# Kernel optimization log

Measured on AMD Instinct MI355X. Metric: run time of the kernel, lower is better.

Reference implementation:

```python
import jax, jax.numpy as jnp
import numpy as np


def setup_inputs() -> dict:
    key = jax.random.key(0)
    k1, k2, k3, k4, k5 = jax.random.split(key, 5)
    B, T, H = 32, 4096, 256
    D = 2 * H  # encoder feature dim
    hidden = jax.random.normal(k1, (B, D), dtype=jnp.float32)
    encoder_outputs = jax.random.normal(k2, (B, T, D), dtype=jnp.float32)
    # torch nn.Linear(4H, H): weight [H, 4H], bias [H]
    W_attn = jax.random.normal(k3, (H, 4 * H), dtype=jnp.float32) * (1.0 / np.sqrt(4 * H))
    b_attn = jax.random.normal(k4, (H,), dtype=jnp.float32) * 0.01
    v = jax.random.uniform(k5, (H,), dtype=jnp.float32)  # torch.rand init
    return {"hidden": hidden, "encoder_outputs": encoder_outputs,
            "W_attn": W_attn, "b_attn": b_attn, "v": v}


def reference(hidden, encoder_outputs, W_attn, b_attn, v):
    D = hidden.shape[-1]  # 2*H
    # Split Linear(4H->H) weight into the hidden part and encoder part so we
    # never materialize the [B,T,4H] concat: cat(h,e) @ W.T == h @ Wh.T + e @ We.T
    W_h = W_attn[:, :D]   # [H, 2H]
    W_e = W_attn[:, D:]   # [H, 2H]
    h_proj = hidden @ W_h.T                     # [B, H]
    e_proj = jnp.einsum('btd,hd->bth', encoder_outputs, W_e)  # [B, T, H]
    energy = jnp.tanh(h_proj[:, None, :] + e_proj + b_attn)   # [B, T, H]
    scores = energy @ v                          # [B, T]
    attn_weights = jax.nn.softmax(scores, axis=1)  # softmax over timesteps
    context = jnp.einsum('bt,btd->bd', attn_weights, encoder_outputs)  # [B, 2H]
    return context, attn_weights
```

## Files before the change

kernel.cpp:

```cpp
#include <hip/hip_runtime.h>
#include <hip/hip_bf16.h>
#include <math.h>

#define B_  32
#define T_  4096
#define H_  256
#define D_  512

#define WS_PRE    0
#define WS_WEHI   32768
#define WS_P      294912
#define WS_ML     819200
#define WS_PCTX   827392

using short8  = __attribute__((ext_vector_type(8))) short;
using float4v = __attribute__((ext_vector_type(4))) float;

__device__ __forceinline__ unsigned cvt2_bf16(float lo, float hi) {
    union { __hip_bfloat162 h; unsigned u; } cv;
    cv.h = __float22bfloat162_rn(make_float2(lo, hi));
    return cv.u;
}
__device__ __forceinline__ short8 cvt8_bf16(const float* a) {
    union { unsigned u[4]; short8 s; } r;
    r.u[0] = cvt2_bf16(a[0], a[1]);
    r.u[1] = cvt2_bf16(a[2], a[3]);
    r.u[2] = cvt2_bf16(a[4], a[5]);
    r.u[3] = cvt2_bf16(a[6], a[7]);
    return r.s;
}

__device__ __forceinline__ float fast_tanh(float x) {
    float e = __expf(2.0f * x);
    return 1.0f - 2.0f * __builtin_amdgcn_rcpf(e + 1.0f);
}

__global__ __launch_bounds__(256)
void prep_kernel(const float* __restrict__ hidden,
                 const float* __restrict__ W_attn,
                 const float* __restrict__ b_attn,
                 unsigned char* __restrict__ ws) {
    int blk = blockIdx.x;
    int tid = threadIdx.x;
    if (blk < 32) {
        int b = blk, h = tid;
        const float4* hv = (const float4*)(hidden + b * D_);
        const float4* wv = (const float4*)(W_attn + (size_t)h * 1024);
        float s = 0.f;
        #pragma unroll 4
        for (int d4 = 0; d4 < D_ / 4; ++d4) {
            float4 a = hv[d4], w = wv[d4];
            s += a.x * w.x + a.y * w.y + a.z * w.z + a.w * w.w;
        }
        ((float*)(ws + WS_PRE))[b * H_ + h] = s + b_attn[h];
    } else {
        int q = (blk - 32) * 256 + tid;
        unsigned short* whi = (unsigned short*)(ws + WS_WEHI);
        #pragma unroll
        for (int i = 0; i < 4; ++i) {
            int idx4 = q + i * 8192;
            int n = idx4 >> 7, k = (idx4 & 127) << 2;
            int t = k >> 5, kin = k & 31;
            int quad = kin >> 3, e = kin & 7;
            int slot = quad ^ ((n >> 1) & 3);
            float4 w = *(const float4*)(W_attn + (size_t)n * 1024 + 512 + k);
            unsigned lo = cvt2_bf16(w.x, w.y);
            unsigned hi = cvt2_bf16(w.z, w.w);
            unsigned short* dst = whi + t * 8192 + n * 32 + slot * 8 + e;
            *(uint2*)dst = make_uint2(lo, hi);
        }
    }
}

#define BM 128
#define BN 256
#define BK 32
#define LDT 40
#define KIT 16

__global__ __launch_bounds__(512, 4)
void gemm_scores_kernel(const float* __restrict__ enc,
                        unsigned char* __restrict__ ws,
                        const float* __restrict__ v) {
    __shared__ unsigned short sA[2][BM * LDT];
    __shared__ unsigned short sB[2][BN * BK];
    __shared__ float sScore[BM];
    __shared__ float sP[BM];
    __shared__ float sRed[4];

    const float*          pre = (const float*)(ws + WS_PRE);
    const unsigned short* weh = (const unsigned short*)(ws + WS_WEHI);

    int tid = threadIdx.x;
    int m0  = blockIdx.x * BM;
    int b   = m0 >> 12;

    if (tid < BM) sScore[tid] = 0.f;

    int rowA = tid & 127, cgA = tid >> 7;
    const float* gA = enc + (size_t)(m0 + rowA) * D_ + cgA * 8;

    int wave = tid >> 6, lane = tid & 63;
    int wm = wave & 1, wn = wave >> 1;
    int quad = lane >> 4, l16 = lane & 15;

    float4v acc[4][4] = {};

    float aX[8], aY[8];

    {
        const float4* p0 = (const float4*)gA;
        float4 x0 = p0[0], x1 = p0[1];
        const uint4* pb0 = (const uint4*)weh;
        uint4 t0 = pb0[tid], t1 = pb0[tid + 512];
        const float4* p1 = (const float4*)(gA + BK);
        float4 y0 = p1[0], y1 = p1[1];

        float tmp[8];
        *(float4*)tmp = x0; *(float4*)(tmp + 4) = x1;
        *(short8*)&sA[0][rowA * LDT + cgA * 8] = cvt8_bf16(tmp);
        ((uint4*)sB[0])[tid]       = t0;
        ((uint4*)sB[0])[tid + 512] = t1;
        *(float4*)aY = y0; *(float4*)(aY + 4) = y1;
    }
    __builtin_amdgcn_s_waitcnt(0xc07f);
    __builtin_amdgcn_s_barrier();

#define K_STEP(kk, CUR, NXT, Acons, Aload)                                    \
    {                                                                         \
        uint4 br0, br1;                                                       \
        if ((kk) + 1 < KIT) {                                                 \
            const uint4* pb = (const uint4*)(weh + ((kk) + 1) * 8192);        \
            br0 = pb[tid]; br1 = pb[tid + 512];                               \
        }                                                                     \
        if ((kk) + 2 < KIT) {                                                 \
            const float4* pa = (const float4*)(gA + ((kk) + 2) * BK);         \
            *(float4*)(Aload) = pa[0]; *(float4*)((Aload) + 4) = pa[1];       \
        }                                                                     \
        short8 ah[4], bh[4];                                                  \
        _Pragma("unroll")                                                     \
        for (int i = 0; i < 4; ++i) {                                         \
            int r = wm * 64 + i * 16 + l16;                                   \
            ah[i] = *(const short8*)&sA[CUR][r * LDT + quad * 8];             \
        }                                                                     \
        _Pragma("unroll")                                                     \
        for (int j = 0; j < 4; ++j) {                                         \
            int c = wn * 64 + j * 16 + l16;                                   \
            int slot = quad ^ ((c >> 1) & 3);                                 \
            bh[j] = *(const short8*)&sB[CUR][c * 32 + slot * 8];              \
        }                                                                     \
        _Pragma("unroll")                                                     \
        for (int i = 0; i < 4; ++i)                                           \
            _Pragma("unroll")                                                 \
            for (int j = 0; j < 4; ++j)                                       \
                acc[i][j] = __builtin_amdgcn_mfma_f32_16x16x32_bf16(          \
                    ah[i], bh[j], acc[i][j], 0, 0, 0);                        \
        if ((kk) + 1 < KIT) {                                                 \
            *(short8*)&sA[NXT][rowA * LDT + cgA * 8] = cvt8_bf16(Acons);      \
            ((uint4*)sB[NXT])[tid]       = br0;                               \
            ((uint4*)sB[NXT])[tid + 512] = br1;                               \
            __builtin_amdgcn_s_waitcnt(0xc07f);                               \
            __builtin_amdgcn_s_barrier();                                     \
        }                                                                     \
    }

    for (int kt = 0; kt < 8; ++kt) {
        K_STEP(2 * kt,     0, 1, aY, aX)
        K_STEP(2 * kt + 1, 1, 0, aX, aY)
    }
#undef K_STEP

    float rowsum[4][4] = {};
    #pragma unroll
    for (int j = 0; j < 4; ++j) {
        int n = wn * 64 + j * 16 + l16;
        float pv = pre[b * H_ + n];
        float vv = v[n];
        #pragma unroll
        for (int i = 0; i < 4; ++i)
            #pragma unroll
            for (int r = 0; r < 4; ++r)
                rowsum[i][r] += fast_tanh(acc[i][j][r] + pv) * vv;
    }
    #pragma unroll
    for (int i = 0; i < 4; ++i)
        #pragma unroll
        for (int r = 0; r < 4; ++r) {
            float s = rowsum[i][r];
            s += __shfl_xor(s, 1);
            s += __shfl_xor(s, 2);
            s += __shfl_xor(s, 4);
            s += __shfl_xor(s, 8);
            rowsum[i][r] = s;
        }
    if (l16 == 0) {
        #pragma unroll
        for (int i = 0; i < 4; ++i)
            #pragma unroll
            for (int r = 0; r < 4; ++r) {
                int row = wm * 64 + i * 16 + quad * 4 + r;
                atomicAdd(&sScore[row], rowsum[i][r]);
            }
    }
    __syncthreads();

    if (tid < 128) {
        float s = sScore[tid];
        float m = s;
        #pragma unroll
        for (int off = 32; off; off >>= 1) m = fmaxf(m, __shfl_xor(m, off));
        if (lane == 0) sRed[wave] = m;
    }
    __syncthreads();
    float m_blk = fmaxf(sRed[0], sRed[1]);
    if (tid < 128) {
        float p = expf(sScore[tid] - m_blk);
        sP[tid] = p;
        ((float*)(ws + WS_P))[m0 + tid] = p;
        float l = p;
        #pragma unroll
        for (int off = 32; off; off >>= 1) l += __shfl_xor(l, off);
        if (lane == 0) sRed[2 + wave] = l;
    }
    __syncthreads();
    if (tid == 0) {
        float2 ml = make_float2(m_blk, sRed[2] + sRed[3]);
        ((float2*)(ws + WS_ML))[blockIdx.x] = ml;
    }

    int colg = tid & 127, rgrp = tid >> 7;
    const float* encb = enc + (size_t)m0 * D_;
    float4 c4 = {0.f, 0.f, 0.f, 0.f};
    #pragma unroll 4
    for (int s = 0; s < 32; ++s) {
        int r = rgrp + 4 * s;
        float w = sP[r];
        float4 ev = *(const float4*)(encb + (size_t)r * D_ + colg * 4);
        c4.x += w * ev.x; c4.y += w * ev.y;
        c4.z += w * ev.z; c4.w += w * ev.w;
    }
    float4* red4 = (float4*)sA;
    red4[tid] = c4;
    __syncthreads();
    if (rgrp == 0) {
        float4 a0 = red4[colg], a1 = red4[colg + 128];
        float4 a2 = red4[colg + 256], a3 = red4[colg + 384];
        float4 o;
        o.x = a0.x + a1.x + a2.x + a3.x;
        o.y = a0.y + a1.y + a2.y + a3.y;
        o.z = a0.z + a1.z + a2.z + a3.z;
        o.w = a0.w + a1.w + a2.w + a3.w;
        ((float4*)(ws + WS_PCTX))[blockIdx.x * 128 + colg] = o;
    }
}

__global__ __launch_bounds__(512)
void finalize_kernel(const unsigned char* __restrict__ ws,
                     float* __restrict__ out_ctx,
                     float* __restrict__ out_w) {
    __shared__ float sm[32], sl[32], sscale[32];
    int b = blockIdx.x, tid = threadIdx.x;
    const float2* ml  = ((const float2*)(ws + WS_ML)) + b * 32;
    if (tid < 32) {
        float2 v = ml[tid];
        sm[tid] = v.x; sl[tid] = v.y;
    }
    __syncthreads();
    float m = -1e30f;
    #pragma unroll
    for (int i = 0; i < 32; ++i) m = fmaxf(m, sm[i]);
    float l = 0.f;
    #pragma unroll
    for (int i = 0; i < 32; ++i) l += sl[i] * expf(sm[i] - m);
    float inv = 1.0f / l;
    if (tid < 32) sscale[tid] = expf(sm[tid] - m) * inv;
    __syncthreads();

    {
        const float4* pb = (const float4*)((const float*)(ws + WS_P) + (size_t)b * T_);
        float4* wb = (float4*)(out_w + (size_t)b * T_);
        int t0 = tid * 2;
        float sc = sscale[tid >> 4];
        float4 x = pb[t0], y = pb[t0 + 1];
        x.x *= sc; x.y *= sc; x.z *= sc; x.w *= sc;
        y.x *= sc; y.y *= sc; y.z *= sc; y.w *= sc;
        wb[t0] = x; wb[t0 + 1] = y;
    }
    {
        const float* pc = (const float*)(ws + WS_PCTX) + (size_t)b * 32 * D_;
        float c = 0.f;
        #pragma unroll
        for (int i = 0; i < 32; ++i) c += pc[i * D_ + tid] * sscale[i];
        out_ctx[b * D_ + tid] = c;
    }
}

extern "C" void kernel_launch(void* const* d_in, const int* in_sizes, int n_in,
                              void* d_out, int out_size, void* d_ws, size_t ws_size,
                              hipStream_t stream) {
    const float* hidden = (const float*)d_in[0];
    const float* enc    = (const float*)d_in[1];
    const float* W_attn = (const float*)d_in[2];
    const float* b_attn = (const float*)d_in[3];
    const float* v      = (const float*)d_in[4];
    float* out = (float*)d_out;
    unsigned char* ws = (unsigned char*)d_ws;

    prep_kernel<<<64, 256, 0, stream>>>(hidden, W_attn, b_attn, ws);
    gemm_scores_kernel<<<T_ * B_ / BM, 512, 0, stream>>>(enc, ws, v);
    finalize_kernel<<<B_, 512, 0, stream>>>(ws, out, out + B_ * D_);
}
```

Measured before the change: 421.4 us.

## Load B fragments directly from global into registers, drop shared-memory B tile

The GEMM no longer stages the pre-swizzled bf16 weight tile through shared memory. Each wave instead loads its MFMA B fragments straight from global (L2-resident) into double-buffered registers, which removes the LDS writes and reads for B and shrinks LDS use, possibly raising occupancy. Score accumulation across the four column-waves now writes per-wave partials to separate LDS slots and sums them instead of using shared atomics. The trade-off is more global load traffic per wave, since each wave re-fetches weights that were previously shared across the block, plus more registers for the B buffers.

```diff
diff --git a/kernel.cpp b/kernel.cpp
--- a/kernel.cpp
+++ b/kernel.cpp
@@ -83,8 +83,7 @@
                         unsigned char* __restrict__ ws,
                         const float* __restrict__ v) {
     __shared__ unsigned short sA[2][BM * LDT];
-    __shared__ unsigned short sB[2][BN * BK];
-    __shared__ float sScore[BM];
+    __shared__ float sScoreP[4][BM];
     __shared__ float sP[BM];
     __shared__ float sRed[4];
 
@@ -95,8 +94,6 @@
     int m0  = blockIdx.x * BM;
     int b   = m0 >> 12;
 
-    if (tid < BM) sScore[tid] = 0.f;
-
     int rowA = tid & 127, cgA = tid >> 7;
     const float* gA = enc + (size_t)(m0 + rowA) * D_ + cgA * 8;
 
@@ -104,69 +101,69 @@
     int wm = wave & 1, wn = wave >> 1;
     int quad = lane >> 4, l16 = lane & 15;
 
+    int slotB = quad ^ ((l16 >> 1) & 3);
+    const unsigned short* bBase = weh + (wn * 64 + l16) * 32 + slotB * 8;
+
     float4v acc[4][4] = {};
 
     float aX[8], aY[8];
+    short8 bhA[4], bhB[4];
 
     {
         const float4* p0 = (const float4*)gA;
         float4 x0 = p0[0], x1 = p0[1];
-        const uint4* pb0 = (const uint4*)weh;
-        uint4 t0 = pb0[tid], t1 = pb0[tid + 512];
+        #pragma unroll
+        for (int j = 0; j < 4; ++j)
+            bhA[j] = *(const short8*)(bBase + j * 512);
         const float4* p1 = (const float4*)(gA + BK);
         float4 y0 = p1[0], y1 = p1[1];
+        #pragma unroll
+        for (int j = 0; j < 4; ++j)
+            bhB[j] = *(const short8*)(bBase + 8192 + j * 512);
 
         float tmp[8];
         *(float4*)tmp = x0; *(float4*)(tmp + 4) = x1;
         *(short8*)&sA[0][rowA * LDT + cgA * 8] = cvt8_bf16(tmp);
-        ((uint4*)sB[0])[tid]       = t0;
-        ((uint4*)sB[0])[tid + 512] = t1;
         *(float4*)aY = y0; *(float4*)(aY + 4) = y1;
     }
     __builtin_amdgcn_s_waitcnt(0xc07f);
     __builtin_amdgcn_s_barrier();
 
-#define K_STEP(kk, CUR, NXT, Acons, Aload)                                    \
+#define K_STEP(kk, CUR, NXT, Acons, Aload, Bcur, Bnxt)                        \
     {                                                                         \
-        uint4 br0, br1;                                                       \
         if ((kk) + 1 < KIT) {                                                 \
-            const uint4* pb = (const uint4*)(weh + ((kk) + 1) * 8192);        \
-            br0 = pb[tid]; br1 = pb[tid + 512];                               \
+            const unsigned short* pb = bBase + ((kk) + 1) * 8192;             \
+            Bnxt[0] = *(const short8*)(pb);                                   \
+            Bnxt[1] = *(const short8*)(pb + 512);                             \
+            Bnxt[2] = *(const short8*)(pb + 1024);                            \
+            Bnxt[3] = *(const short8*)(pb + 1536);                            \
         }                                                                     \
         if ((kk) + 2 < KIT) {                                                 \
             const float4* pa = (const float4*)(gA + ((kk) + 2) * BK);         \
             *(float4*)(Aload) = pa[0]; *(float4*)((Aload) + 4) = pa[1];       \
         }                                                                     \
-        short8 ah[4], bh[4];                                                  \
+        short8 ah[4];                                                         \
         _Pragma("unroll")                                                     \
         for (int i = 0; i < 4; ++i) {                                         \
             int r = wm * 64 + i * 16 + l16;                                   \
             ah[i] = *(const short8*)&sA[CUR][r * LDT + quad * 8];             \
         }                                                                     \
         _Pragma("unroll")                                                     \
-        for (int j = 0; j < 4; ++j) {                                         \
-            int c = wn * 64 + j * 16 + l16;                                   \
-            int slot = quad ^ ((c >> 1) & 3);                                 \
-            bh[j] = *(const short8*)&sB[CUR][c * 32 + slot * 8];              \
-        }                                                                     \
-        _Pragma("unroll")                                                     \
         for (int i = 0; i < 4; ++i)                                           \
             _Pragma("unroll")                                                 \
             for (int j = 0; j < 4; ++j)                                       \
                 acc[i][j] = __builtin_amdgcn_mfma_f32_16x16x32_bf16(          \
-                    ah[i], bh[j], acc[i][j], 0, 0, 0);                        \
+                    ah[i], Bcur[j], acc[i][j], 0, 0, 0);                      \
         if ((kk) + 1 < KIT) {                                                 \
             *(short8*)&sA[NXT][rowA * LDT + cgA * 8] = cvt8_bf16(Acons);      \
-            ((uint4*)sB[NXT])[tid]       = br0;                               \
-            ((uint4*)sB[NXT])[tid + 512] = br1;                               \
             __builtin_amdgcn_s_waitcnt(0xc07f);                               \
             __builtin_amdgcn_s_barrier();                                     \
         }                                                                     \
     }
 
     for (int kt = 0; kt < 8; ++kt) {
-        K_STEP(2 * kt,     0, 1, aY, aX)
-        K_STEP(2 * kt + 1, 1, 0, aX, aY)
+        K_STEP(2 * kt,     0, 1, aY, aX, bhA, bhB)
+        K_STEP(2 * kt + 1, 1, 0, aX, aY, bhB, bhA)
     }
 #undef K_STEP
 
@@ -199,14 +196,16 @@
             #pragma unroll
             for (int r = 0; r < 4; ++r) {
                 int row = wm * 64 + i * 16 + quad * 4 + r;
-                atomicAdd(&sScore[row], rowsum[i][r]);
+                sScoreP[wn][row] = rowsum[i][r];
             }
     }
     __syncthreads();
 
+    float sval = 0.f;
     if (tid < 128) {
-        float s = sScore[tid];
-        float m = s;
+        sval = sScoreP[0][tid] + sScoreP[1][tid]
+             + sScoreP[2][tid] + sScoreP[3][tid];
+        float m = sval;
         #pragma unroll
         for (int off = 32; off; off >>= 1) m = fmaxf(m, __shfl_xor(m, off));
         if (lane == 0) sRed[wave] = m;
@@ -214,7 +213,7 @@
     __syncthreads();
     float m_blk = fmaxf(sRed[0], sRed[1]);
     if (tid < 128) {
-        float p = expf(sScore[tid] - m_blk);
+        float p = expf(sval - m_blk);
         sP[tid] = p;
         ((float*)(ws + WS_P))[m0 + tid] = p;
         float l = p;
```

Result: no change. 419.3 us, median of 2 (-0.5%).
